# Optimization experiments

Hardware: AMD Instinct MI355X
Metric: run time of the kernel (lower is better)

The kernel has to match this reference:

```python
import jax, jax.numpy as jnp
import numpy as np

B, L, D = 4, 4096, 1024
EPS_NORM = 1e-6
EPS_PHAZOR = 1e-5


def setup_inputs() -> dict:
    key = jax.random.key(0)
    ks = jax.random.split(key, 8)
    gain = 0.01 * np.sqrt(2.0 / (D + D))  # xavier_normal_ with gain=0.01 for dim x dim
    inp = {
        "x": jax.random.normal(ks[0], (B, L, D), dtype=jnp.float32),
        "Wz": (jax.random.normal(ks[1], (D, D), dtype=jnp.float32) * gain),
        "bz": jnp.zeros((D,), jnp.float32),
        "Wza": (jax.random.normal(ks[2], (D, D), dtype=jnp.float32) * gain),
        "bza": jnp.zeros((D,), jnp.float32),
        "Wy": (jax.random.normal(ks[3], (D, D), dtype=jnp.float32) * gain),
        "by": jnp.zeros((D,), jnp.float32),
        "Wya": (jax.random.normal(ks[4], (D, D), dtype=jnp.float32) * gain),
        "bya": jnp.zeros((D,), jnp.float32),
        "norm_w": jnp.ones((D,), jnp.float32),
        "lc_re": jax.random.normal(ks[5], (D,), dtype=jnp.float32),  # last_conv_init real part
        "lc_im": jax.random.normal(ks[6], (D,), dtype=jnp.float32),  # last_conv_init imag part
    }
    return inp


def reference(x, Wz, bz, Wza, bza, Wy, by, Wya, bya, norm_w, lc_re, lc_im):
    b, l, d = x.shape
    # phazor_angle_scale = 0.001 ** linspace(0,1,d) (non-trainable buffer)
    scale = jnp.power(jnp.float32(0.001), jnp.linspace(0.0, 1.0, d, dtype=jnp.float32))
    ln_phazor = EPS_PHAZOR + 1j * scale.astype(jnp.complex64)  # (d,) complex64

    # gated input projection: z = fc_z(x) * silu(fc_z_act(x))
    z = (x @ Wz.T + bz) * jax.nn.silu(x @ Wza.T + bza)
    z = z.astype(jnp.complex64)  # (b, l, d)

    # phazor progression exp(l * ln_phazor), (l, d) complex
    t = jnp.arange(l, dtype=jnp.float32)
    phazor_prog = jnp.exp(t[:, None].astype(jnp.complex64) * ln_phazor[None, :])

    # causal diagonal linear recurrence via zero-padded FFT conv along seq
    phazor_fft = jnp.fft.fft(phazor_prog, n=2 * l, axis=0)          # (2l, d)
    z_fft = jnp.fft.fft(z, n=2 * l, axis=1)                          # (b, 2l, d)
    h_inner = jnp.fft.ifft(z_fft * phazor_fft[None], axis=1)[:, :l]  # (b, l, d)

    # carry-in from previous chunk state: last_conv * phazor_prog * exp(ln_phazor)
    last_conv = (lc_re + 1j * lc_im).astype(jnp.complex64)           # (d,)
    h_cross = last_conv[None, None, :] * (phazor_prog * jnp.exp(ln_phazor)[None, :])[None]

    h = (h_inner + h_cross).real  # (b, l, d) float32

    # RMSNorm(h) then gated output projection
    normed = h * jax.lax.rsqrt(jnp.mean(h * h, axis=-1, keepdims=True) + EPS_NORM) * norm_w
    y = (normed @ Wy.T + by) * jax.nn.silu(x @ Wya.T + bya)
    return y
```

## Files before the change

### kernel.cpp

```cpp
#include <hip/hip_runtime.h>

typedef unsigned short u16;
using bf16x8 = __attribute__((ext_vector_type(8))) __bf16;
using f32x4  = __attribute__((ext_vector_type(4))) float;

#define GL_TO_LDS(gp, sp) \
  __builtin_amdgcn_global_load_lds((const __attribute__((address_space(1))) void*)(gp), \
                                   (__attribute__((address_space(3))) void*)(sp), 16, 0, 0)

__device__ __forceinline__ u16 f2bf(float f){
  unsigned u = __builtin_bit_cast(unsigned, f);
  u += 0x7fffu + ((u >> 16) & 1u);
  return (u16)(u >> 16);
}

constexpr int SB = 4, SL = 4096, SD = 1024;
constexpr int GM = SB * SL, GN = SD, GK = SD;
constexpr int NCHUNK = 64, CH = SL / NCHUNK;
constexpr float EPS_PHAZOR = 1e-5f;
constexpr float LOG2_SCALE = -9.965784284662087f;

__global__ __launch_bounds__(256) void k_convert(
    const float4* __restrict__ x4, const float4* __restrict__ wz4,
    const float4* __restrict__ wza4, const float4* __restrict__ wy4,
    const float4* __restrict__ wya4, u16* __restrict__ xb, u16* __restrict__ wb){
  int gid = blockIdx.x * 256 + threadIdx.x;
  const float4* src; u16* dst;
  if (gid < (GM * GK / 8)){
    src = x4 + (size_t)gid * 2; dst = xb + (size_t)gid * 8;
  } else {
    int g2 = gid - GM * GK / 8;
    int which = g2 >> 17, off = g2 & 0x1ffff;
    const float4* s4 = which == 0 ? wz4 : which == 1 ? wza4 : which == 2 ? wy4 : wya4;
    src = s4 + (size_t)off * 2; dst = wb + (size_t)which * (GK * GN) + (size_t)off * 8;
  }
  float4 a = src[0], b = src[1];
  u16 r[8] = {f2bf(a.x), f2bf(a.y), f2bf(a.z), f2bf(a.w),
              f2bf(b.x), f2bf(b.y), f2bf(b.z), f2bf(b.w)};
  *reinterpret_cast<uint4*>(dst) = *reinterpret_cast<const uint4*>(r);
}

template<bool SAME_A>
__global__ __launch_bounds__(256, 2) void k_gemm_dual(
    const u16* __restrict__ A0, const u16* __restrict__ A1,
    const u16* __restrict__ W0, const u16* __restrict__ W1,
    const float* __restrict__ bias0, const float* __restrict__ bias1,
    float* __restrict__ out){
  __shared__ u16 sA0[128][32];
  __shared__ u16 sB0[128][32];
  __shared__ u16 sB1[128][32];
  __shared__ u16 sA1[SAME_A ? 4 : 128][32];

  const int tid  = threadIdx.x;
  const int wave = tid >> 6, lane = tid & 63;
  const int wm = wave >> 1, wn = wave & 1;
  const int lr = lane & 15, lg = lane >> 4;
  const int bm = blockIdx.y, bn = blockIdx.x;

  const int r0 = tid >> 2, s0 = tid & 3;
  const int c1 = 256 + tid;
  const int r1 = c1 >> 2, s1 = c1 & 3;
  const int sp0 = (wave * 64) * 8;
  const int sp1 = (256 + wave * 64) * 8;

  f32x4 acc0[4][4] = {};
  f32x4 acc1[4][4] = {};

  for (int k0 = 0; k0 < GK; k0 += 32){
    {
      const u16* g;
      g = A0 + (size_t)(bm * 128 + r0) * GK + k0 + s0 * 8; GL_TO_LDS(g, &sA0[0][0] + sp0);
      g = A0 + (size_t)(bm * 128 + r1) * GK + k0 + s1 * 8; GL_TO_LDS(g, &sA0[0][0] + sp1);
      g = W0 + (size_t)(bn * 128 + r0) * GK + k0 + s0 * 8; GL_TO_LDS(g, &sB0[0][0] + sp0);
      g = W0 + (size_t)(bn * 128 + r1) * GK + k0 + s1 * 8; GL_TO_LDS(g, &sB0[0][0] + sp1);
      g = W1 + (size_t)(bn * 128 + r0) * GK + k0 + s0 * 8; GL_TO_LDS(g, &sB1[0][0] + sp0);
      g = W1 + (size_t)(bn * 128 + r1) * GK + k0 + s1 * 8; GL_TO_LDS(g, &sB1[0][0] + sp1);
      if constexpr(!SAME_A){
        g = A1 + (size_t)(bm * 128 + r0) * GK + k0 + s0 * 8; GL_TO_LDS(g, &sA1[0][0] + sp0);
        g = A1 + (size_t)(bm * 128 + r1) * GK + k0 + s1 * 8; GL_TO_LDS(g, &sA1[0][0] + sp1);
      }
    }
    __syncthreads();

    bf16x8 a0f[4], b0f[4], b1f[4], a1f[4];
    #pragma unroll
    for (int f = 0; f < 4; f++){
      a0f[f] = *reinterpret_cast<const bf16x8*>(&sA0[wm * 64 + f * 16 + lr][lg * 8]);
      b0f[f] = *reinterpret_cast<const bf16x8*>(&sB0[wn * 64 + f * 16 + lr][lg * 8]);
      b1f[f] = *reinterpret_cast<const bf16x8*>(&sB1[wn * 64 + f * 16 + lr][lg * 8]);
      if constexpr(!SAME_A)
        a1f[f] = *reinterpret_cast<const bf16x8*>(&sA1[wm * 64 + f * 16 + lr][lg * 8]);
    }
    #pragma unroll
    for (int mf = 0; mf < 4; mf++){
      #pragma unroll
      for (int nf = 0; nf < 4; nf++){
        acc0[mf][nf] = __builtin_amdgcn_mfma_f32_16x16x32_bf16(a0f[mf], b0f[nf], acc0[mf][nf], 0, 0, 0);
        if constexpr(SAME_A)
          acc1[mf][nf] = __builtin_amdgcn_mfma_f32_16x16x32_bf16(a0f[mf], b1f[nf], acc1[mf][nf], 0, 0, 0);
        else
          acc1[mf][nf] = __builtin_amdgcn_mfma_f32_16x16x32_bf16(a1f[mf], b1f[nf], acc1[mf][nf], 0, 0, 0);
      }
    }
    __syncthreads();
  }

  #pragma unroll
  for (int nf = 0; nf < 4; nf++){
    const int col = bn * 128 + wn * 64 + nf * 16 + lr;
    const float bb0 = bias0[col], bb1 = bias1[col];
    #pragma unroll
    for (int mf = 0; mf < 4; mf++){
      const int rowb = bm * 128 + wm * 64 + mf * 16 + lg * 4;
      f32x4 v0 = acc0[mf][nf], v1 = acc1[mf][nf];
      #pragma unroll
      for (int r = 0; r < 4; r++){
        float p0 = v0[r] + bb0, p1 = v1[r] + bb1;
        float sg = p1 / (1.f + __expf(-p1));
        out[(size_t)(rowb + r) * GN + col] = p0 * sg;
      }
    }
  }
}

__global__ __launch_bounds__(256) void k_scan1(const float* __restrict__ z, float2* __restrict__ carry){
  const int d = blockIdx.x * 256 + threadIdx.x;
  const int c = blockIdx.y, b = blockIdx.z;
  const float sc = exp2f(LOG2_SCALE * ((float)d * (1.0f / 1023.0f)));
  float si, co; sincosf(sc, &si, &co);
  const float er = expf(EPS_PHAZOR);
  const float rre = er * co, rim = er * si;
  const float* zp = z + ((size_t)b * SL + (size_t)c * CH) * SD + d;
  float hre = 0.f, him = 0.f;
  #pragma unroll 8
  for (int i = 0; i < CH; i++){
    float zv = zp[i * SD];
    float nr = fmaf(rre, hre, fmaf(-rim, him, zv));
    him = fmaf(rre, him, rim * hre);
    hre = nr;
  }
  carry[(size_t)(b * NCHUNK + c) * SD + d] = make_float2(hre, him);
}

__global__ __launch_bounds__(256) void k_scan2(const float2* __restrict__ carry,
    const float* __restrict__ lcre, const float* __restrict__ lcim, float2* __restrict__ hin){
  const int idx = blockIdx.x * 256 + threadIdx.x;
  const int b = idx >> 10, d = idx & 1023;
  const float sc = exp2f(LOG2_SCALE * ((float)d * (1.0f / 1023.0f)));
  float si, co; sincosf((float)CH * sc, &si, &co);
  const float eC = expf((float)CH * EPS_PHAZOR);
  const float Rre = eC * co, Rim = eC * si;
  float hre = lcre[d], him = lcim[d];
  for (int c = 0; c < NCHUNK; c++){
    const size_t o = (size_t)(b * NCHUNK + c) * SD + d;
    hin[o] = make_float2(hre, him);
    float2 cv = carry[o];
    float nr = fmaf(Rre, hre, fmaf(-Rim, him, cv.x));
    him = fmaf(Rre, him, fmaf(Rim, hre, cv.y));
    hre = nr;
  }
}

__global__ __launch_bounds__(256) void k_scan3(float* __restrict__ zh, const float2* __restrict__ hin){
  const int d = blockIdx.x * 256 + threadIdx.x;
  const int c = blockIdx.y, b = blockIdx.z;
  const float sc = exp2f(LOG2_SCALE * ((float)d * (1.0f / 1023.0f)));
  float si, co; sincosf(sc, &si, &co);
  const float er = expf(EPS_PHAZOR);
  const float rre = er * co, rim = er * si;
  float2 h0 = hin[(size_t)(b * NCHUNK + c) * SD + d];
  float hre = h0.x, him = h0.y;
  float* zp = zh + ((size_t)b * SL + (size_t)c * CH) * SD + d;
  #pragma unroll 8
  for (int i = 0; i < CH; i++){
    float zv = zp[i * SD];
    float nr = fmaf(rre, hre, fmaf(-rim, him, zv));
    him = fmaf(rre, him, rim * hre);
    hre = nr;
    zp[i * SD] = hre;
  }
}

__global__ __launch_bounds__(256) void k_rmsnorm(const float* __restrict__ h,
    const float* __restrict__ nw, u16* __restrict__ outb){
  const int row = blockIdx.x, tid = threadIdx.x;
  const float4 v = reinterpret_cast<const float4*>(h + (size_t)row * SD)[tid];
  float ss = v.x * v.x + v.y * v.y + v.z * v.z + v.w * v.w;
  #pragma unroll
  for (int o = 32; o; o >>= 1) ss += __shfl_down(ss, o, 64);
  __shared__ float red[5];
  const int lane = tid & 63, wid = tid >> 6;
  if (lane == 0) red[wid] = ss;
  __syncthreads();
  if (tid == 0) red[4] = rsqrtf((red[0] + red[1] + red[2] + red[3]) * (1.0f / (float)SD) + 1e-6f);
  __syncthreads();
  const float inv = red[4];
  const float4 w = reinterpret_cast<const float4*>(nw)[tid];
  u16 r[4] = { f2bf(v.x * inv * w.x), f2bf(v.y * inv * w.y),
               f2bf(v.z * inv * w.z), f2bf(v.w * inv * w.w) };
  reinterpret_cast<ushort4*>(outb + (size_t)row * SD)[tid] = *reinterpret_cast<const ushort4*>(r);
}

extern "C" void kernel_launch(void* const* d_in, const int* in_sizes, int n_in,
                              void* d_out, int out_size, void* d_ws, size_t ws_size,
                              hipStream_t stream){
  const float* x    = (const float*)d_in[0];
  const float* Wz   = (const float*)d_in[1];
  const float* bz   = (const float*)d_in[2];
  const float* Wza  = (const float*)d_in[3];
  const float* bza  = (const float*)d_in[4];
  const float* Wy   = (const float*)d_in[5];
  const float* by   = (const float*)d_in[6];
  const float* Wya  = (const float*)d_in[7];
  const float* bya  = (const float*)d_in[8];
  const float* nw   = (const float*)d_in[9];
  const float* lcre = (const float*)d_in[10];
  const float* lcim = (const float*)d_in[11];

  char* ws = (char*)d_ws;
  u16*    xb      = (u16*)(ws);
  u16*    wb      = (u16*)(ws + (32ull << 20));
  u16*    normedb = (u16*)(ws + (40ull << 20));
  float2* carry   = (float2*)(ws + (40ull << 20));
  float2* hin     = (float2*)(ws + (42ull << 20));
  float*  zbuf    = (float*)(ws + (72ull << 20));
  float*  y       = (float*)d_out;

  k_convert<<<10240, 256, 0, stream>>>((const float4*)x, (const float4*)Wz, (const float4*)Wza,
                                       (const float4*)Wy, (const float4*)Wya, xb, wb);
  k_gemm_dual<true ><<<dim3(GN / 128, GM / 128), 256, 0, stream>>>(
      xb, xb, wb, wb + (size_t)GK * GN, bz, bza, zbuf);
  k_scan1<<<dim3(SD / 256, NCHUNK, SB), 256, 0, stream>>>(zbuf, carry);
  k_scan2<<<(SB * SD) / 256, 256, 0, stream>>>(carry, lcre, lcim, hin);
  k_scan3<<<dim3(SD / 256, NCHUNK, SB), 256, 0, stream>>>(zbuf, hin);
  k_rmsnorm<<<GM, 256, 0, stream>>>(zbuf, nw, normedb);
  k_gemm_dual<false><<<dim3(GN / 128, GM / 128), 256, 0, stream>>>(
      normedb, xb, wb + 2ull * GK * GN, wb + 3ull * GK * GN, by, bya, y);
}
```

Before: 386.1 us.

## Replace dual GEMMs with 256x256 pipelined single GEMMs and bf16 intermediates

Replaces the 128x128 dual-weight GEMM with a 512-thread 256x256-tile GEMM using K=64 steps, double-buffered global-to-LDS loads, an XOR-swizzled LDS layout and setprio around MFMA groups. The gates are computed as separate GEMMs and stored in bf16, then fused into the epilogue of the later GEMMs. The z/h intermediate buffer is stored in bf16 instead of fp32, which halves scan and rmsnorm traffic. In exchange there are four GEMM launches instead of two, extra gate-tensor round trips, and precision loss in the recurrence input and output.

```diff
diff --git a/kernel.cpp b/kernel.cpp
--- a/kernel.cpp
+++ b/kernel.cpp
@@ -13,9 +13,14 @@
   u += 0x7fffu + ((u >> 16) & 1u);
   return (u16)(u >> 16);
 }
+__device__ __forceinline__ float bf2f(u16 v){
+  unsigned u = ((unsigned)v) << 16;
+  return __builtin_bit_cast(float, u);
+}
 
 constexpr int SB = 4, SL = 4096, SD = 1024;
 constexpr int GM = SB * SL, GN = SD, GK = SD;
+constexpr int NT = GK / 64;
 constexpr int NCHUNK = 64, CH = SL / NCHUNK;
 constexpr float EPS_PHAZOR = 1e-5f;
 constexpr float LOG2_SCALE = -9.965784284662087f;
@@ -40,101 +45,131 @@
   *reinterpret_cast<uint4*>(dst) = *reinterpret_cast<const uint4*>(r);
 }
 
-template<bool SAME_A>
-__global__ __launch_bounds__(256, 2) void k_gemm_dual(
-    const u16* __restrict__ A0, const u16* __restrict__ A1,
-    const u16* __restrict__ W0, const u16* __restrict__ W1,
-    const float* __restrict__ bias0, const float* __restrict__ bias1,
-    float* __restrict__ out){
-  __shared__ u16 sA0[128][32];
-  __shared__ u16 sB0[128][32];
-  __shared__ u16 sB1[128][32];
-  __shared__ u16 sA1[SAME_A ? 4 : 128][32];
-
-  const int tid  = threadIdx.x;
-  const int wave = tid >> 6, lane = tid & 63;
-  const int wm = wave >> 1, wn = wave & 1;
-  const int lr = lane & 15, lg = lane >> 4;
+#define LDA(dst, q, pk) { _Pragma("unroll") for (int mf = 0; mf < 4; ++mf) \
+  dst[mf] = *reinterpret_cast<const bf16x8*>(&lds[abase + ((q)*64 + mf*16)*64 + (pk)*8]); }
+#define LDB(dst, pk) { _Pragma("unroll") for (int nf = 0; nf < 4; ++nf) \
+  dst[nf] = *reinterpret_cast<const bf16x8*>(&lds[bbase + (nf*16)*64 + (pk)*8]); }
+#define MM(qq, af, bfr) { _Pragma("unroll") for (int mf = 0; mf < 4; ++mf) \
+  _Pragma("unroll") for (int nf = 0; nf < 4; ++nf) \
+    acc[(qq)*4+mf][nf] = __builtin_amdgcn_mfma_f32_16x16x32_bf16(af[mf], bfr[nf], acc[(qq)*4+mf][nf], 0, 0, 0); }
+
+template<int MODE>
+__global__ __launch_bounds__(512, 2) void k_gemm8(
+    const u16* __restrict__ A, const u16* __restrict__ W,
+    const float* __restrict__ bias, const u16* __restrict__ gate,
+    void* __restrict__ outp){
+  __shared__ u16 lds[65536];
+
+  const int tid = threadIdx.x;
+  const int w = tid >> 6, ln = tid & 63;
+  const int wm = w >> 2, wn = w & 3;
+  const int lr = ln & 15, lg = ln >> 4;
   const int bm = blockIdx.y, bn = blockIdx.x;
 
-  const int r0 = tid >> 2, s0 = tid & 3;
-  const int c1 = 256 + tid;
-  const int r1 = c1 >> 2, s1 = c1 & 3;
-  const int sp0 = (wave * 64) * 8;
-  const int sp1 = (256 + wave * 64) * 8;
-
-  f32x4 acc0[4][4] = {};
-  f32x4 acc1[4][4] = {};
-
-  for (int k0 = 0; k0 < GK; k0 += 32){
-    {
-      const u16* g;
-      g = A0 + (size_t)(bm * 128 + r0) * GK + k0 + s0 * 8; GL_TO_LDS(g, &sA0[0][0] + sp0);
-      g = A0 + (size_t)(bm * 128 + r1) * GK + k0 + s1 * 8; GL_TO_LDS(g, &sA0[0][0] + sp1);
-      g = W0 + (size_t)(bn * 128 + r0) * GK + k0 + s0 * 8; GL_TO_LDS(g, &sB0[0][0] + sp0);
-      g = W0 + (size_t)(bn * 128 + r1) * GK + k0 + s1 * 8; GL_TO_LDS(g, &sB0[0][0] + sp1);
-      g = W1 + (size_t)(bn * 128 + r0) * GK + k0 + s0 * 8; GL_TO_LDS(g, &sB1[0][0] + sp0);
-      g = W1 + (size_t)(bn * 128 + r1) * GK + k0 + s1 * 8; GL_TO_LDS(g, &sB1[0][0] + sp1);
-      if constexpr(!SAME_A){
-        g = A1 + (size_t)(bm * 128 + r0) * GK + k0 + s0 * 8; GL_TO_LDS(g, &sA1[0][0] + sp0);
-        g = A1 + (size_t)(bm * 128 + r1) * GK + k0 + s1 * 8; GL_TO_LDS(g, &sA1[0][0] + sp1);
+  const int r0 = tid >> 3;
+  const int l8 = ((tid & 7) ^ (r0 & 7)) * 8;
+  const u16* Arow = A + (size_t)(bm * 256) * GK + l8;
+  const u16* Wrow = W + (size_t)(bn * 256) * GK + l8;
+  const u16* srcs[8];
+  srcs[0] = Arow + (size_t)(r0      ) * GK;
+  srcs[1] = Arow + (size_t)(r0 +  64) * GK;
+  srcs[2] = Arow + (size_t)(r0 + 128) * GK;
+  srcs[3] = Arow + (size_t)(r0 + 192) * GK;
+  srcs[4] = Wrow + (size_t)(r0      ) * GK;
+  srcs[5] = Wrow + (size_t)(r0 +  64) * GK;
+  srcs[6] = Wrow + (size_t)(r0 + 128) * GK;
+  srcs[7] = Wrow + (size_t)(r0 + 192) * GK;
+  int dstb[8];
+  dstb[0] = 0     + w * 512;  dstb[1] = 4096  + w * 512;
+  dstb[2] = 8192  + w * 512;  dstb[3] = 12288 + w * 512;
+  dstb[4] = 32768 + w * 512;  dstb[5] = 36864 + w * 512;
+  dstb[6] = 40960 + w * 512;  dstb[7] = 45056 + w * 512;
+
+  const int pk0 = lg ^ (lr & 7);
+  const int pk1 = (4 + lg) ^ (lr & 7);
+
+  f32x4 acc[8][4] = {};
+
+  {
+    #pragma unroll
+    for (int u = 0; u < 8; ++u) GL_TO_LDS(srcs[u], &lds[dstb[u]]);
+    asm volatile("s_waitcnt vmcnt(0)" ::: "memory");
+    __builtin_amdgcn_s_barrier();
+  }
+
+  for (int t = 0; t < NT; ++t){
+    const int sl = t & 1;
+    const int abase = sl * 16384 + wm * 8192 + lr * 64;
+    const int bbase = 32768 + sl * 16384 + (wn >> 1) * 8192 + ((wn & 1) * 64 + lr) * 64;
+    bf16x8 a0[4], a1[4], b0[4], b1[4];
+
+    LDA(a0, 0, pk0); LDB(b0, pk0);
+    if (t + 1 < NT){
+      const int sb = (sl ^ 1) * 16384;
+      #pragma unroll
+      for (int u = 0; u < 8; ++u) GL_TO_LDS(srcs[u] + (t + 1) * 64, &lds[dstb[u] + sb]);
+    }
+    __builtin_amdgcn_s_setprio(1); MM(0, a0, b0); __builtin_amdgcn_s_setprio(0);
+    __builtin_amdgcn_s_barrier();
+    LDA(a1, 1, pk0);
+    __builtin_amdgcn_s_setprio(1); MM(1, a1, b0); __builtin_amdgcn_s_setprio(0);
+    __builtin_amdgcn_s_barrier();
+    LDA(a0, 0, pk1); LDB(b1, pk1);
+    __builtin_amdgcn_s_setprio(1); MM(0, a0, b1); __builtin_amdgcn_s_setprio(0);
+    __builtin_amdgcn_s_barrier();
+    LDA(a1, 1, pk1);
+    __builtin_amdgcn_s_setprio(1); MM(1, a1, b1); __builtin_amdgcn_s_setprio(0);
+    if (t + 1 < NT) asm volatile("s_waitcnt vmcnt(0)" ::: "memory");
+    __builtin_amdgcn_s_barrier();
+  }
+
+  #pragma unroll
+  for (int nf = 0; nf < 4; ++nf){
+    const int col = bn * 256 + wn * 64 + nf * 16 + lr;
+    const float bb = bias[col];
+    #pragma unroll
+    for (int ri = 0; ri < 8; ++ri){
+      const int rowb = bm * 256 + wm * 128 + ri * 16 + lg * 4;
+      f32x4 v = acc[ri][nf];
+      if constexpr(MODE == 0){
+        u16* gout = (u16*)outp;
+        #pragma unroll
+        for (int r = 0; r < 4; ++r){
+          float p = v[r] + bb;
+          float s = p / (1.f + __expf(-p));
+          gout[(size_t)(rowb + r) * GN + col] = f2bf(s);
+        }
+      } else if constexpr(MODE == 1){
+        float* fout = (float*)outp;
+        #pragma unroll
+        for (int r = 0; r < 4; ++r){
+          float g = bf2f(gate[(size_t)(rowb + r) * GN + col]);
+          fout[(size_t)(rowb + r) * GN + col] = (v[r] + bb) * g;
+        }
+      } else {
+        u16* zout = (u16*)outp;
+        #pragma unroll
+        for (int r = 0; r < 4; ++r){
+          float g = bf2f(gate[(size_t)(rowb + r) * GN + col]);
+          zout[(size_t)(rowb + r) * GN + col] = f2bf((v[r] + bb) * g);
+        }
       }
     }
-    __syncthreads();
-
-    bf16x8 a0f[4], b0f[4], b1f[4], a1f[4];
-    #pragma unroll
-    for (int f = 0; f < 4; f++){
-      a0f[f] = *reinterpret_cast<const bf16x8*>(&sA0[wm * 64 + f * 16 + lr][lg * 8]);
-      b0f[f] = *reinterpret_cast<const bf16x8*>(&sB0[wn * 64 + f * 16 + lr][lg * 8]);
-      b1f[f] = *reinterpret_cast<const bf16x8*>(&sB1[wn * 64 + f * 16 + lr][lg * 8]);
-      if constexpr(!SAME_A)
-        a1f[f] = *reinterpret_cast<const bf16x8*>(&sA1[wm * 64 + f * 16 + lr][lg * 8]);
-    }
-    #pragma unroll
-    for (int mf = 0; mf < 4; mf++){
-      #pragma unroll
-      for (int nf = 0; nf < 4; nf++){
-        acc0[mf][nf] = __builtin_amdgcn_mfma_f32_16x16x32_bf16(a0f[mf], b0f[nf], acc0[mf][nf], 0, 0, 0);
-        if constexpr(SAME_A)
-          acc1[mf][nf] = __builtin_amdgcn_mfma_f32_16x16x32_bf16(a0f[mf], b1f[nf], acc1[mf][nf], 0, 0, 0);
-        else
-          acc1[mf][nf] = __builtin_amdgcn_mfma_f32_16x16x32_bf16(a1f[mf], b1f[nf], acc1[mf][nf], 0, 0, 0);
-      }
-    }
-    __syncthreads();
-  }
-
-  #pragma unroll
-  for (int nf = 0; nf < 4; nf++){
-    const int col = bn * 128 + wn * 64 + nf * 16 + lr;
-    const float bb0 = bias0[col], bb1 = bias1[col];
-    #pragma unroll
-    for (int mf = 0; mf < 4; mf++){
-      const int rowb = bm * 128 + wm * 64 + mf * 16 + lg * 4;
-      f32x4 v0 = acc0[mf][nf], v1 = acc1[mf][nf];
-      #pragma unroll
-      for (int r = 0; r < 4; r++){
-        float p0 = v0[r] + bb0, p1 = v1[r] + bb1;
-        float sg = p1 / (1.f + __expf(-p1));
-        out[(size_t)(rowb + r) * GN + col] = p0 * sg;
-      }
-    }
-  }
-}
-
-__global__ __launch_bounds__(256) void k_scan1(const float* __restrict__ z, float2* __restrict__ carry){
+  }
+}
+
+__global__ __launch_bounds__(256) void k_scan1(const u16* __restrict__ z, float2* __restrict__ carry){
   const int d = blockIdx.x * 256 + threadIdx.x;
   const int c = blockIdx.y, b = blockIdx.z;
   const float sc = exp2f(LOG2_SCALE * ((float)d * (1.0f / 1023.0f)));
   float si, co; sincosf(sc, &si, &co);
   const float er = expf(EPS_PHAZOR);
   const float rre = er * co, rim = er * si;
-  const float* zp = z + ((size_t)b * SL + (size_t)c * CH) * SD + d;
+  const u16* zp = z + ((size_t)b * SL + (size_t)c * CH) * SD + d;
   float hre = 0.f, him = 0.f;
   #pragma unroll 8
   for (int i = 0; i < CH; i++){
-    float zv = zp[i * SD];
+    float zv = bf2f(zp[i * SD]);
     float nr = fmaf(rre, hre, fmaf(-rim, him, zv));
     him = fmaf(rre, him, rim * hre);
     hre = nr;
@@ -161,7 +196,7 @@
   }
 }
 
-__global__ __launch_bounds__(256) void k_scan3(float* __restrict__ zh, const float2* __restrict__ hin){
+__global__ __launch_bounds__(256) void k_scan3(u16* __restrict__ zh, const float2* __restrict__ hin){
   const int d = blockIdx.x * 256 + threadIdx.x;
   const int c = blockIdx.y, b = blockIdx.z;
   const float sc = exp2f(LOG2_SCALE * ((float)d * (1.0f / 1023.0f)));
@@ -170,22 +205,23 @@
   const float rre = er * co, rim = er * si;
   float2 h0 = hin[(size_t)(b * NCHUNK + c) * SD + d];
   float hre = h0.x, him = h0.y;
-  float* zp = zh + ((size_t)b * SL + (size_t)c * CH) * SD + d;
+  u16* zp = zh + ((size_t)b * SL + (size_t)c * CH) * SD + d;
   #pragma unroll 8
   for (int i = 0; i < CH; i++){
-    float zv = zp[i * SD];
+    float zv = bf2f(zp[i * SD]);
     float nr = fmaf(rre, hre, fmaf(-rim, him, zv));
     him = fmaf(rre, him, rim * hre);
     hre = nr;
-    zp[i * SD] = hre;
-  }
-}
-
-__global__ __launch_bounds__(256) void k_rmsnorm(const float* __restrict__ h,
+    zp[i * SD] = f2bf(hre);
+  }
+}
+
+__global__ __launch_bounds__(256) void k_rmsnorm(const u16* __restrict__ h,
     const float* __restrict__ nw, u16* __restrict__ outb){
   const int row = blockIdx.x, tid = threadIdx.x;
-  const float4 v = reinterpret_cast<const float4*>(h + (size_t)row * SD)[tid];
-  float ss = v.x * v.x + v.y * v.y + v.z * v.z + v.w * v.w;
+  const ushort4 hv = reinterpret_cast<const ushort4*>(h + (size_t)row * SD)[tid];
+  float v0 = bf2f(hv.x), v1 = bf2f(hv.y), v2 = bf2f(hv.z), v3 = bf2f(hv.w);
+  float ss = v0 * v0 + v1 * v1 + v2 * v2 + v3 * v3;
   #pragma unroll
   for (int o = 32; o; o >>= 1) ss += __shfl_down(ss, o, 64);
   __shared__ float red[5];
@@ -196,8 +232,8 @@
   __syncthreads();
   const float inv = red[4];
   const float4 w = reinterpret_cast<const float4*>(nw)[tid];
-  u16 r[4] = { f2bf(v.x * inv * w.x), f2bf(v.y * inv * w.y),
-               f2bf(v.z * inv * w.z), f2bf(v.w * inv * w.w) };
+  u16 r[4] = { f2bf(v0 * inv * w.x), f2bf(v1 * inv * w.y),
+               f2bf(v2 * inv * w.z), f2bf(v3 * inv * w.w) };
   reinterpret_cast<ushort4*>(outb + (size_t)row * SD)[tid] = *reinterpret_cast<const ushort4*>(r);
 }
 
@@ -219,21 +255,26 @@
 
   char* ws = (char*)d_ws;
   u16*    xb      = (u16*)(ws);
+  u16*    normedb = (u16*)(ws);
   u16*    wb      = (u16*)(ws + (32ull << 20));
-  u16*    normedb = (u16*)(ws + (40ull << 20));
+  u16*    gz      = (u16*)(ws + (40ull << 20));
   float2* carry   = (float2*)(ws + (40ull << 20));
   float2* hin     = (float2*)(ws + (42ull << 20));
-  float*  zbuf    = (float*)(ws + (72ull << 20));
+  u16*    gy      = (u16*)(ws + (72ull << 20));
+  u16*    zb      = (u16*)(ws + (104ull << 20));
   float*  y       = (float*)d_out;
+
+  const size_t WSZ = (size_t)GK * GN;
+  dim3 ggrid(GN / 256, GM / 256);
 
   k_convert<<<10240, 256, 0, stream>>>((const float4*)x, (const float4*)Wz, (const float4*)Wza,
                                        (const float4*)Wy, (const float4*)Wya, xb, wb);
-  k_gemm_dual<true ><<<dim3(GN / 128, GM / 128), 256, 0, stream>>>(
-      xb, xb, wb, wb + (size_t)GK * GN, bz, bza, zbuf);
-  k_scan1<<<dim3(SD / 256, NCHUNK, SB), 256, 0, stream>>>(zbuf, carry);
+  k_gemm8<0><<<ggrid, 512, 0, stream>>>(xb, wb + 3 * WSZ, bya, nullptr, gy);
+  k_gemm8<0><<<ggrid, 512, 0, stream>>>(xb, wb + 1 * WSZ, bza, nullptr, gz);
+  k_gemm8<2><<<ggrid, 512, 0, stream>>>(xb, wb + 0 * WSZ, bz, gz, zb);
+  k_scan1<<<dim3(SD / 256, NCHUNK, SB), 256, 0, stream>>>(zb, carry);
   k_scan2<<<(SB * SD) / 256, 256, 0, stream>>>(carry, lcre, lcim, hin);
-  k_scan3<<<dim3(SD / 256, NCHUNK, SB), 256, 0, stream>>>(zbuf, hin);
-  k_rmsnorm<<<GM, 256, 0, stream>>>(zbuf, nw, normedb);
-  k_gemm_dual<false><<<dim3(GN / 128, GM / 128), 256, 0, stream>>>(
-      normedb, xb, wb + 2ull * GK * GN, wb + 3ull * GK * GN, by, bya, y);
-}
+  k_scan3<<<dim3(SD / 256, NCHUNK, SB), 256, 0, stream>>>(zb, hin);
+  k_rmsnorm<<<GM, 256, 0, stream>>>(zb, nw, normedb);
+  k_gemm8<1><<<ggrid, 512, 0, stream>>>(normedb, wb + 2 * WSZ, by, gy, y);
+}
```

Result: slower. 421.1 us (+9.1%).
